# Performance work log

Measured on AMD Instinct MI355X. Metric: run time of the kernel, lower is better.

Reference implementation:

```python
import jax, jax.numpy as jnp
import numpy as np

EMBED_DIM = 512
KERNEL = 17


def setup_inputs() -> dict:
    key = jax.random.key(0)
    ks = jax.random.split(key, 5)
    B, L, C = 2, 8192, EMBED_DIM
    s = C ** -0.5
    x = jax.random.normal(ks[0], (B, L, C), dtype=jnp.float32)
    # weights stored as (in, out); equivalent to torch Linear weight.T
    w_qkv = jax.random.normal(ks[1], (C, 3 * C), dtype=jnp.float32) * s
    w_width = jax.random.normal(ks[2], (C, 1), dtype=jnp.float32) * s
    b_width = jax.random.normal(ks[3], (1,), dtype=jnp.float32) * 0.01
    w_out = jax.random.normal(ks[4], (C, C), dtype=jnp.float32) * s
    return {"x": x, "w_qkv": w_qkv, "w_width": w_width, "b_width": b_width, "w_out": w_out}


def reference(x, w_qkv, w_width, b_width, w_out):
    B, L, C = x.shape
    K = KERNEL
    half_k = K // 2
    scale = C ** -0.5

    qkv = x @ w_qkv                      # [B,L,3C]
    q, k, v = jnp.split(qkv, 3, axis=-1)

    # learned soft window width in [1, K]
    width = jax.nn.sigmoid(x @ w_width + b_width) * (K - 1) + 1.0   # [B,L,1]

    # sliding windows of k/v: pad along L then gather K-sized windows
    k_pad = jnp.pad(k, ((0, 0), (half_k, half_k), (0, 0)))
    v_pad = jnp.pad(v, ((0, 0), (half_k, half_k), (0, 0)))
    idx = jnp.arange(L)[:, None] + jnp.arange(K)[None, :]           # [L,K]
    k_win = k_pad[:, idx]                # [B,L,K,C]
    v_win = v_pad[:, idx]                # [B,L,K,C]

    scores = jnp.einsum('blc,blkc->blk', q, k_win) * scale          # [B,L,K]

    rel_pos = jnp.abs(jnp.arange(K, dtype=jnp.float32) - half_k)    # [K]
    soft_mask = jax.nn.sigmoid((width - rel_pos) * 5.0)             # [B,L,K]
    scores = scores - (1.0 - soft_mask) * 10000.0

    attn = jax.nn.softmax(scores, axis=-1)
    out = jnp.einsum('blk,blkc->blc', attn, v_win)                  # [B,L,C]
    return (out + v) @ w_out
```

## Files before the change

kernel.cpp:

```cpp
#include <hip/hip_runtime.h>

typedef unsigned short u16;
typedef unsigned int   u32;
typedef __attribute__((ext_vector_type(8))) short          shortx8;
typedef __attribute__((ext_vector_type(8))) unsigned short ushortx8;
typedef __attribute__((ext_vector_type(4))) float          floatx4;

#define AS1 __attribute__((address_space(1)))
#define AS3 __attribute__((address_space(3)))

#define SEG 8208
#define LV  16416

__device__ __forceinline__ float b2f(u16 v) {
  return __uint_as_float(((u32)v) << 16);
}
__device__ __forceinline__ u16 f2b(float f) {
  u32 u = __float_as_uint(f);
  u += 0x7FFF + ((u >> 16) & 1);
  return (u16)(u >> 16);
}
__device__ __forceinline__ void cp16(const void* g, void* l) {
  __builtin_amdgcn_global_load_lds((AS1 u32*)g, (AS3 u32*)l, 16, 0, 0);
}

__global__ void transpose_cast(const float* __restrict__ in, u16* __restrict__ out,
                               int R, int C) {
  __shared__ u16 tile[32][33];
  const int tx = threadIdx.x & 31;
  const int ty = threadIdx.x >> 5;
  const int cb = blockIdx.x * 32;
  const int rb = blockIdx.y * 32;
#pragma unroll
  for (int i = 0; i < 32; i += 8)
    tile[ty + i][tx] = f2b(in[(size_t)(rb + ty + i) * C + cb + tx]);
  __syncthreads();
#pragma unroll
  for (int i = 0; i < 32; i += 8)
    out[(size_t)(cb + ty + i) * R + rb + tx] = tile[tx][ty + i];
}

__global__ __launch_bounds__(256)
void cast_width(const float* __restrict__ x, const float* __restrict__ w_width,
                const float* __restrict__ b_width, u16* __restrict__ xb,
                float* __restrict__ width) {
  const int lane = threadIdx.x & 63;
  const int row  = blockIdx.x * 4 + (threadIdx.x >> 6);
  const float* xp = x + (size_t)row * 512 + lane * 8;
  floatx4 v0 = *(const floatx4*)xp;
  floatx4 v1 = *(const floatx4*)(xp + 4);
  floatx4 w0 = *(const floatx4*)(w_width + lane * 8);
  floatx4 w1 = *(const floatx4*)(w_width + lane * 8 + 4);
  float s = 0.f;
  ushortx8 o;
#pragma unroll
  for (int j = 0; j < 4; ++j) {
    s += v0[j] * w0[j] + v1[j] * w1[j];
    o[j] = f2b(v0[j]); o[4 + j] = f2b(v1[j]);
  }
  *(ushortx8*)(xb + (size_t)row * 512 + lane * 8) = o;
#pragma unroll
  for (int m = 32; m >= 1; m >>= 1) s += __shfl_xor(s, m, 64);
  if (lane == 0)
    width[row] = 16.f / (1.f + __expf(-(s + b_width[0]))) + 1.f;
}

__global__ void vt_zero_pad(u16* __restrict__ Vt) {
  const int idx = blockIdx.x * 256 + threadIdx.x;
  const int ch = idx >> 5;
  const int k  = idx & 31;
  const int seg = k >> 4;
  const int j   = k & 15;
  const int col = seg * SEG + (j < 8 ? j : 8192 + j);
  Vt[(size_t)ch * LV + col] = 0;
}

template <int MODE>
__global__ __launch_bounds__(256, 2)
void gemm_bt(const u16* __restrict__ A, const u16* __restrict__ Bt,
             void* __restrict__ C0, u16* __restrict__ Kb, u16* __restrict__ Vt) {
  const int K = 512;
  __shared__ alignas(16) u16 lds[17408];
  u16* As = lds;
  u16* Bs = lds + 8192;
  const int tid  = threadIdx.x;
  const int lane = tid & 63;
  const int wave = tid >> 6;
  const int quad = lane >> 4;
  const int lr   = lane & 15;
  const int row0 = blockIdx.x * 128;
  const int col0 = blockIdx.y * 128;
  const int wr   = (wave >> 1) * 64;
  const int wc   = (wave & 1) * 64;

  floatx4 acc[4][4];
#pragma unroll
  for (int i = 0; i < 4; ++i)
#pragma unroll
    for (int j = 0; j < 4; ++j) acc[i][j] = (floatx4)0.0f;

  int srow[4], scol[4];
#pragma unroll
  for (int p = 0; p < 4; ++p) {
    int c = p * 256 + tid;
    srow[p] = c >> 3;
    scol[p] = ((c & 7) ^ (srow[p] & 7)) * 8;
  }
  const int swz = lr & 7;

  for (int k0 = 0; k0 < K; k0 += 64) {
#pragma unroll
    for (int p = 0; p < 4; ++p)
      cp16(A + (size_t)(row0 + srow[p]) * K + k0 + scol[p], &As[(p * 256 + tid) * 8]);
#pragma unroll
    for (int p = 0; p < 4; ++p)
      cp16(Bt + (size_t)(col0 + srow[p]) * K + k0 + scol[p], &Bs[(p * 256 + tid) * 8]);
    __syncthreads();

#pragma unroll
    for (int ks = 0; ks < 2; ++ks) {
      shortx8 af[4], bf[4];
#pragma unroll
      for (int mi = 0; mi < 4; ++mi)
        af[mi] = *(const shortx8*)
            &As[((wr + mi * 16 + lr) * 8 + ((ks * 4 + quad) ^ swz)) * 8];
#pragma unroll
      for (int ni = 0; ni < 4; ++ni)
        bf[ni] = *(const shortx8*)
            &Bs[((wc + ni * 16 + lr) * 8 + ((ks * 4 + quad) ^ swz)) * 8];
#pragma unroll
      for (int mi = 0; mi < 4; ++mi)
#pragma unroll
        for (int ni = 0; ni < 4; ++ni)
          acc[mi][ni] = __builtin_amdgcn_mfma_f32_16x16x32_bf16(
              af[mi], bf[ni], acc[mi][ni], 0, 0, 0);
    }
    __syncthreads();
  }

  if constexpr (MODE == 1) {
    if (col0 < 1024) {
      u16* dst = (col0 < 512) ? (u16*)C0 : Kb;
      const int cb = col0 & 511;
#pragma unroll
      for (int mi = 0; mi < 4; ++mi)
#pragma unroll
        for (int ni = 0; ni < 4; ++ni)
#pragma unroll
          for (int r = 0; r < 4; ++r)
            lds[(wr + mi * 16 + quad * 4 + r) * 136 + wc + ni * 16 + lr] =
                f2b(acc[mi][ni][r]);
      __syncthreads();
      const int rr = tid >> 4, cc = (tid & 15) * 8;
#pragma unroll
      for (int it = 0; it < 8; ++it) {
        int row = it * 16 + rr;
        *(ushortx8*)(dst + (size_t)(row0 + row) * 512 + cb + cc) =
            *(const ushortx8*)&lds[row * 136 + cc];
      }
    } else {
      const int cb = col0 - 1024;
      const int bb = row0 >> 13, pib0 = row0 & 8191;
#pragma unroll
      for (int mi = 0; mi < 4; ++mi)
#pragma unroll
        for (int ni = 0; ni < 4; ++ni)
#pragma unroll
          for (int r = 0; r < 4; ++r)
            lds[(wc + ni * 16 + lr) * 136 + wr + mi * 16 + quad * 4 + r] =
                f2b(acc[mi][ni][r]);
      __syncthreads();
      const int rr = tid >> 4, cc = (tid & 15) * 8;
#pragma unroll
      for (int it = 0; it < 8; ++it) {
        int chl = it * 16 + rr;
        ushortx8 v = *(const ushortx8*)&lds[chl * 136 + cc];
        *(ushortx8*)(Vt + (size_t)(cb + chl) * LV + (size_t)bb * SEG + 8 + pib0 + cc) = v;
      }
    }
  } else {
    float* Cf = (float*)C0;
#pragma unroll
    for (int mi = 0; mi < 4; ++mi)
#pragma unroll
      for (int ni = 0; ni < 4; ++ni)
#pragma unroll
        for (int r = 0; r < 4; ++r) {
          int row = row0 + wr + mi * 16 + quad * 4 + r;
          int col = col0 + wc + ni * 16 + lr;
          Cf[(size_t)row * 512 + col] = acc[mi][ni][r];
        }
  }
}

__global__ __launch_bounds__(256)
void attn_mfma(const u16* __restrict__ Q, const u16* __restrict__ Kb,
               const u16* __restrict__ Vt, const float* __restrict__ width,
               u16* __restrict__ Out) {
  __shared__ float Sp[8][16][16];
  __shared__ u16   P[16][32];
  __shared__ u16   O[4][16][128];
  const int tid  = threadIdx.x;
  const int lane = tid & 63;
  const int wave = tid >> 6;
  const int quad = lane >> 4;
  const int lr   = lane & 15;
  const int p0   = blockIdx.x * 16;
  const int pib0 = p0 & 8191;
  const int bb   = p0 >> 13;

  floatx4 s0 = (floatx4)0.0f, s1 = (floatx4)0.0f;
#pragma unroll
  for (int s = 0; s < 4; ++s) {
    const int k0 = wave * 128 + s * 32 + quad * 8;
    shortx8 af = *(const shortx8*)(Q  + (size_t)(p0 + lr) * 512 + k0);
    shortx8 f0 = *(const shortx8*)(Kb + (ptrdiff_t)(p0 - 8 + lr) * 512 + k0);
    shortx8 f1 = *(const shortx8*)(Kb + (ptrdiff_t)(p0 + 8 + lr) * 512 + k0);
    s0 = __builtin_amdgcn_mfma_f32_16x16x32_bf16(af, f0, s0, 0, 0, 0);
    s1 = __builtin_amdgcn_mfma_f32_16x16x32_bf16(af, f1, s1, 0, 0, 0);
  }
#pragma unroll
  for (int r = 0; r < 4; ++r) {
    Sp[wave * 2 + 0][quad * 4 + r][lr] = s0[r];
    Sp[wave * 2 + 1][quad * 4 + r][lr] = s1[r];
  }
  __syncthreads();

  {
    const int row = tid >> 4, cg = tid & 15;
    const float scale = 0.044194173824159216f;
    const float wrow  = width[p0 + row];
    float sv[2]; float mx = -1e30f;
#pragma unroll
    for (int t = 0; t < 2; ++t) {
      const int col = t * 16 + cg;
      float s = Sp[t][row][cg] + Sp[2 + t][row][cg] +
                Sp[4 + t][row][cg] + Sp[6 + t][row][cg];
      const int d  = col - row;
      const int jb = pib0 + col - 8;
      const bool inband  = (d >= 0) && (d <= 16);
      const bool inbatch = ((unsigned)jb < 8192u);
      float rel  = fabsf((float)(d - 8));
      float mask = 1.f / (1.f + __expf(-5.f * (wrow - rel)));
      float pen  = (1.f - mask) * 10000.f;
      float val  = inband ? ((inbatch ? s * scale : 0.f) - pen) : -1e30f;
      sv[t] = val;
      mx = fmaxf(mx, val);
    }
#pragma unroll
    for (int m = 8; m >= 1; m >>= 1) mx = fmaxf(mx, __shfl_xor(mx, m, 64));
    float e0 = __expf(sv[0] - mx), e1 = __expf(sv[1] - mx);
    float sum = e0 + e1;
#pragma unroll
    for (int m = 8; m >= 1; m >>= 1) sum += __shfl_xor(sum, m, 64);
    const float inv = 1.f / sum;
    P[row][cg]      = f2b(e0 * inv + ((cg - row) == 8 ? 1.f : 0.f));
    P[row][cg + 16] = f2b(e1 * inv + ((cg + 16 - row) == 8 ? 1.f : 0.f));
  }
  __syncthreads();

  shortx8 pf = *(const shortx8*)&P[lr][quad * 8];
  const size_t cb0 = (size_t)bb * SEG + pib0;
#pragma unroll
  for (int ct = 0; ct < 8; ++ct) {
    const int ch = wave * 128 + ct * 16 + lr;
    shortx8 vf = *(const shortx8*)(Vt + (size_t)ch * LV + cb0 + quad * 8);
    floatx4 o = __builtin_amdgcn_mfma_f32_16x16x32_bf16(pf, vf, (floatx4)0.0f,
                                                        0, 0, 0);
#pragma unroll
    for (int r = 0; r < 4; ++r)
      O[wave][quad * 4 + r][ct * 16 + lr] = f2b(o[r]);
  }
  __syncthreads();
  {
    const int orow = lane >> 2;
#pragma unroll
    for (int i = 0; i < 4; ++i) {
      const int c = i * 32 + (lane & 3) * 8;
      ushortx8 v = *(const ushortx8*)&O[wave][orow][c];
      *(ushortx8*)(Out + (size_t)(p0 + orow) * 512 + wave * 128 + c) = v;
    }
  }
}

extern "C" void kernel_launch(void* const* d_in, const int* in_sizes, int n_in,
                              void* d_out, int out_size, void* d_ws, size_t ws_size,
                              hipStream_t stream) {
  const float* x       = (const float*)d_in[0];
  const float* w_qkv   = (const float*)d_in[1];
  const float* w_width = (const float*)d_in[2];
  const float* b_width = (const float*)d_in[3];
  const float* w_out   = (const float*)d_in[4];
  float* out = (float*)d_out;

  const int M = 16384, C = 512, N3 = 1536;
  char* ws = (char*)d_ws;
  u16*   xb    = (u16*)(ws);
  u16*   Qb    = (u16*)(ws + 16777216);
  u16*   Kb    = (u16*)(ws + 33554432 + 8192);
  u16*   Vt    = (u16*)(ws + 50348032);
  u16*   wqkvT = (u16*)(ws + 67158016);
  u16*   woutT = (u16*)(ws + 68730880);
  float* width = (float*)(ws + 69255168);

  dim3 blk(256);
  vt_zero_pad<<<dim3(64), blk, 0, stream>>>(Vt);
  cast_width<<<dim3(M / 4), blk, 0, stream>>>(x, w_width, b_width, xb, width);
  transpose_cast<<<dim3(N3 / 32, C / 32), blk, 0, stream>>>(w_qkv, wqkvT, C, N3);
  transpose_cast<<<dim3(C / 32, C / 32), blk, 0, stream>>>(w_out, woutT, C, C);
  gemm_bt<1><<<dim3(M / 128, N3 / 128), blk, 0, stream>>>(xb, wqkvT, Qb, Kb, Vt);
  attn_mfma<<<dim3(M / 16), blk, 0, stream>>>(Qb, Kb, Vt, width, Qb);
  gemm_bt<2><<<dim3(M / 128, C / 128), blk, 0, stream>>>(Qb, woutT, out, nullptr, nullptr);
}
```

Measured before the change: 160.5 us.

## Fuse prep kernels, raise GEMM occupancy, compute attention scores per-wave redundantly

Merges the zero-pad, cast/width, and two weight transpose kernels into one launch to cut launch overhead. Raises the GEMM launch bound to 4 blocks per CU, which may force register spills. In attention, each wave now computes the full 512-channel QK scores itself and does the softmax in registers with shuffles. This removes the cross-wave LDS reduction and one barrier, but quadruples the QK loads and MFMAs, and it pads the LDS arrays to avoid bank conflicts.

After: 165.4 us. 3.0% more time.

```diff
diff --git a/kernel.cpp b/kernel.cpp
--- a/kernel.cpp
+++ b/kernel.cpp
@@ -24,59 +24,63 @@
   __builtin_amdgcn_global_load_lds((AS1 u32*)g, (AS3 u32*)l, 16, 0, 0);
 }
 
-__global__ void transpose_cast(const float* __restrict__ in, u16* __restrict__ out,
-                               int R, int C) {
+__global__ __launch_bounds__(256)
+void prep(const float* __restrict__ x, const float* __restrict__ w_width,
+          const float* __restrict__ b_width, const float* __restrict__ w_qkv,
+          const float* __restrict__ w_out, u16* __restrict__ xb,
+          float* __restrict__ width, u16* __restrict__ wqkvT,
+          u16* __restrict__ woutT, u16* __restrict__ Vt) {
   __shared__ u16 tile[32][33];
-  const int tx = threadIdx.x & 31;
-  const int ty = threadIdx.x >> 5;
-  const int cb = blockIdx.x * 32;
-  const int rb = blockIdx.y * 32;
-#pragma unroll
-  for (int i = 0; i < 32; i += 8)
-    tile[ty + i][tx] = f2b(in[(size_t)(rb + ty + i) * C + cb + tx]);
-  __syncthreads();
-#pragma unroll
-  for (int i = 0; i < 32; i += 8)
-    out[(size_t)(cb + ty + i) * R + rb + tx] = tile[tx][ty + i];
-}
-
-__global__ __launch_bounds__(256)
-void cast_width(const float* __restrict__ x, const float* __restrict__ w_width,
-                const float* __restrict__ b_width, u16* __restrict__ xb,
-                float* __restrict__ width) {
-  const int lane = threadIdx.x & 63;
-  const int row  = blockIdx.x * 4 + (threadIdx.x >> 6);
-  const float* xp = x + (size_t)row * 512 + lane * 8;
-  floatx4 v0 = *(const floatx4*)xp;
-  floatx4 v1 = *(const floatx4*)(xp + 4);
-  floatx4 w0 = *(const floatx4*)(w_width + lane * 8);
-  floatx4 w1 = *(const floatx4*)(w_width + lane * 8 + 4);
-  float s = 0.f;
-  ushortx8 o;
-#pragma unroll
-  for (int j = 0; j < 4; ++j) {
-    s += v0[j] * w0[j] + v1[j] * w1[j];
-    o[j] = f2b(v0[j]); o[4 + j] = f2b(v1[j]);
-  }
-  *(ushortx8*)(xb + (size_t)row * 512 + lane * 8) = o;
-#pragma unroll
-  for (int m = 32; m >= 1; m >>= 1) s += __shfl_xor(s, m, 64);
-  if (lane == 0)
-    width[row] = 16.f / (1.f + __expf(-(s + b_width[0]))) + 1.f;
-}
-
-__global__ void vt_zero_pad(u16* __restrict__ Vt) {
-  const int idx = blockIdx.x * 256 + threadIdx.x;
-  const int ch = idx >> 5;
-  const int k  = idx & 31;
-  const int seg = k >> 4;
-  const int j   = k & 15;
-  const int col = seg * SEG + (j < 8 ? j : 8192 + j);
-  Vt[(size_t)ch * LV + col] = 0;
+  const int b = blockIdx.x;
+  if (b < 4096) {
+    const int lane = threadIdx.x & 63;
+    const int row  = b * 4 + (threadIdx.x >> 6);
+    const float* xp = x + (size_t)row * 512 + lane * 8;
+    floatx4 v0 = *(const floatx4*)xp;
+    floatx4 v1 = *(const floatx4*)(xp + 4);
+    floatx4 w0 = *(const floatx4*)(w_width + lane * 8);
+    floatx4 w1 = *(const floatx4*)(w_width + lane * 8 + 4);
+    float s = 0.f;
+    ushortx8 o;
+#pragma unroll
+    for (int j = 0; j < 4; ++j) {
+      s += v0[j] * w0[j] + v1[j] * w1[j];
+      o[j] = f2b(v0[j]); o[4 + j] = f2b(v1[j]);
+    }
+    *(ushortx8*)(xb + (size_t)row * 512 + lane * 8) = o;
+#pragma unroll
+    for (int m = 32; m >= 1; m >>= 1) s += __shfl_xor(s, m, 64);
+    if (lane == 0)
+      width[row] = 16.f / (1.f + __expf(-(s + b_width[0]))) + 1.f;
+  } else if (b < 5120) {
+    const float* in; u16* out; int R, C, t;
+    if (b < 4864) { in = w_qkv; out = wqkvT; R = 512; C = 1536; t = b - 4096; }
+    else          { in = w_out; out = woutT; R = 512; C = 512;  t = b - 4864; }
+    const int nbx = C / 32;
+    const int cb = (t % nbx) * 32;
+    const int rb = (t / nbx) * 32;
+    const int tx = threadIdx.x & 31;
+    const int ty = threadIdx.x >> 5;
+#pragma unroll
+    for (int i = 0; i < 32; i += 8)
+      tile[ty + i][tx] = f2b(in[(size_t)(rb + ty + i) * C + cb + tx]);
+    __syncthreads();
+#pragma unroll
+    for (int i = 0; i < 32; i += 8)
+      out[(size_t)(cb + ty + i) * R + rb + tx] = tile[tx][ty + i];
+  } else {
+    const int idx = (b - 5120) * 256 + threadIdx.x;
+    const int ch = idx >> 5;
+    const int k  = idx & 31;
+    const int seg = k >> 4;
+    const int j   = k & 15;
+    const int col = seg * SEG + (j < 8 ? j : 8192 + j);
+    Vt[(size_t)ch * LV + col] = 0;
+  }
 }
 
 template <int MODE>
-__global__ __launch_bounds__(256, 2)
+__global__ __launch_bounds__(256, 4)
 void gemm_bt(const u16* __restrict__ A, const u16* __restrict__ Bt,
              void* __restrict__ C0, u16* __restrict__ Kb, u16* __restrict__ Vt) {
   const int K = 512;
@@ -197,9 +201,8 @@
 void attn_mfma(const u16* __restrict__ Q, const u16* __restrict__ Kb,
                const u16* __restrict__ Vt, const float* __restrict__ width,
                u16* __restrict__ Out) {
-  __shared__ float Sp[8][16][16];
-  __shared__ u16   P[16][32];
-  __shared__ u16   O[4][16][128];
+  __shared__ u16 P[4][16][40];
+  __shared__ u16 O[4][16][136];
   const int tid  = threadIdx.x;
   const int lane = tid & 63;
   const int wave = tid >> 6;
@@ -211,55 +214,68 @@
 
   floatx4 s0 = (floatx4)0.0f, s1 = (floatx4)0.0f;
 #pragma unroll
-  for (int s = 0; s < 4; ++s) {
-    const int k0 = wave * 128 + s * 32 + quad * 8;
+  for (int s = 0; s < 16; ++s) {
+    const int k0 = s * 32 + quad * 8;
     shortx8 af = *(const shortx8*)(Q  + (size_t)(p0 + lr) * 512 + k0);
     shortx8 f0 = *(const shortx8*)(Kb + (ptrdiff_t)(p0 - 8 + lr) * 512 + k0);
     shortx8 f1 = *(const shortx8*)(Kb + (ptrdiff_t)(p0 + 8 + lr) * 512 + k0);
     s0 = __builtin_amdgcn_mfma_f32_16x16x32_bf16(af, f0, s0, 0, 0, 0);
     s1 = __builtin_amdgcn_mfma_f32_16x16x32_bf16(af, f1, s1, 0, 0, 0);
   }
+
+  const float scale = 0.044194173824159216f;
+  float v0[4], v1[4], mx[4];
 #pragma unroll
   for (int r = 0; r < 4; ++r) {
-    Sp[wave * 2 + 0][quad * 4 + r][lr] = s0[r];
-    Sp[wave * 2 + 1][quad * 4 + r][lr] = s1[r];
-  }
-  __syncthreads();
-
-  {
-    const int row = tid >> 4, cg = tid & 15;
-    const float scale = 0.044194173824159216f;
-    const float wrow  = width[p0 + row];
-    float sv[2]; float mx = -1e30f;
-#pragma unroll
-    for (int t = 0; t < 2; ++t) {
-      const int col = t * 16 + cg;
-      float s = Sp[t][row][cg] + Sp[2 + t][row][cg] +
-                Sp[4 + t][row][cg] + Sp[6 + t][row][cg];
-      const int d  = col - row;
-      const int jb = pib0 + col - 8;
-      const bool inband  = (d >= 0) && (d <= 16);
+    const int row = quad * 4 + r;
+    const float wrow = width[p0 + row];
+    {
+      const int d  = lr - row;
+      const int jb = pib0 + lr - 8;
+      const bool inband  = (d >= 0);
       const bool inbatch = ((unsigned)jb < 8192u);
       float rel  = fabsf((float)(d - 8));
       float mask = 1.f / (1.f + __expf(-5.f * (wrow - rel)));
       float pen  = (1.f - mask) * 10000.f;
-      float val  = inband ? ((inbatch ? s * scale : 0.f) - pen) : -1e30f;
-      sv[t] = val;
-      mx = fmaxf(mx, val);
-    }
-#pragma unroll
-    for (int m = 8; m >= 1; m >>= 1) mx = fmaxf(mx, __shfl_xor(mx, m, 64));
-    float e0 = __expf(sv[0] - mx), e1 = __expf(sv[1] - mx);
-    float sum = e0 + e1;
-#pragma unroll
-    for (int m = 8; m >= 1; m >>= 1) sum += __shfl_xor(sum, m, 64);
-    const float inv = 1.f / sum;
-    P[row][cg]      = f2b(e0 * inv + ((cg - row) == 8 ? 1.f : 0.f));
-    P[row][cg + 16] = f2b(e1 * inv + ((cg + 16 - row) == 8 ? 1.f : 0.f));
+      v0[r] = inband ? ((inbatch ? s0[r] * scale : 0.f) - pen) : -1e30f;
+    }
+    {
+      const int d  = lr + 16 - row;
+      const int jb = pib0 + lr + 8;
+      const bool inband  = (d <= 16);
+      const bool inbatch = ((unsigned)jb < 8192u);
+      float rel  = fabsf((float)(d - 8));
+      float mask = 1.f / (1.f + __expf(-5.f * (wrow - rel)));
+      float pen  = (1.f - mask) * 10000.f;
+      v1[r] = inband ? ((inbatch ? s1[r] * scale : 0.f) - pen) : -1e30f;
+    }
+    mx[r] = fmaxf(v0[r], v1[r]);
+  }
+#pragma unroll
+  for (int m = 8; m >= 1; m >>= 1)
+#pragma unroll
+    for (int r = 0; r < 4; ++r) mx[r] = fmaxf(mx[r], __shfl_xor(mx[r], m, 64));
+  float e0[4], e1[4], sum[4];
+#pragma unroll
+  for (int r = 0; r < 4; ++r) {
+    e0[r] = __expf(v0[r] - mx[r]);
+    e1[r] = __expf(v1[r] - mx[r]);
+    sum[r] = e0[r] + e1[r];
+  }
+#pragma unroll
+  for (int m = 8; m >= 1; m >>= 1)
+#pragma unroll
+    for (int r = 0; r < 4; ++r) sum[r] += __shfl_xor(sum[r], m, 64);
+#pragma unroll
+  for (int r = 0; r < 4; ++r) {
+    const int row = quad * 4 + r;
+    const float inv = 1.f / sum[r];
+    P[wave][row][lr]      = f2b(e0[r] * inv + ((lr - row) == 8 ? 1.f : 0.f));
+    P[wave][row][lr + 16] = f2b(e1[r] * inv + ((lr + 16 - row) == 8 ? 1.f : 0.f));
   }
   __syncthreads();
 
-  shortx8 pf = *(const shortx8*)&P[lr][quad * 8];
+  shortx8 pf = *(const shortx8*)&P[wave][lr][quad * 8];
   const size_t cb0 = (size_t)bb * SEG + pib0;
 #pragma unroll
   for (int ct = 0; ct < 8; ++ct) {
@@ -304,10 +320,8 @@
   float* width = (float*)(ws + 69255168);
 
   dim3 blk(256);
-  vt_zero_pad<<<dim3(64), blk, 0, stream>>>(Vt);
-  cast_width<<<dim3(M / 4), blk, 0, stream>>>(x, w_width, b_width, xb, width);
-  transpose_cast<<<dim3(N3 / 32, C / 32), blk, 0, stream>>>(w_qkv, wqkvT, C, N3);
-  transpose_cast<<<dim3(C / 32, C / 32), blk, 0, stream>>>(w_out, woutT, C, C);
+  prep<<<dim3(5184), blk, 0, stream>>>(x, w_width, b_width, w_qkv, w_out,
+                                       xb, width, wqkvT, woutT, Vt);
   gemm_bt<1><<<dim3(M / 128, N3 / 128), blk, 0, stream>>>(xb, wqkvT, Qb, Kb, Vt);
   attn_mfma<<<dim3(M / 16), blk, 0, stream>>>(Qb, Kb, Vt, width, Qb);
   gemm_bt<2><<<dim3(M / 128, C / 128), blk, 0, stream>>>(Qb, woutT, out, nullptr, nullptr);
```

## Fuse prep kernels into one launch, raise GEMM occupancy, pad attention LDS

Applied to the files above, without the earlier changes.

Merges the four preprocessing kernels (Vt zero-padding, x cast plus width, and both weight transpose-casts) into one launch that picks its branch by block index. This removes three kernel launches and the gaps between them. The GEMM launch bound minimum-blocks hint rises from 2 to 3 to push occupancy, which may constrain register allocation. The attention output LDS buffer row is padded from 128 to 136 elements to reduce bank conflicts.

New measurement: 152.4 us, median of 2. -5.1%, faster.

```diff
diff --git a/kernel.cpp b/kernel.cpp
--- a/kernel.cpp
+++ b/kernel.cpp
@@ -24,59 +24,63 @@
   __builtin_amdgcn_global_load_lds((AS1 u32*)g, (AS3 u32*)l, 16, 0, 0);
 }
 
-__global__ void transpose_cast(const float* __restrict__ in, u16* __restrict__ out,
-                               int R, int C) {
+__global__ __launch_bounds__(256)
+void prep(const float* __restrict__ x, const float* __restrict__ w_width,
+          const float* __restrict__ b_width, const float* __restrict__ w_qkv,
+          const float* __restrict__ w_out, u16* __restrict__ xb,
+          float* __restrict__ width, u16* __restrict__ wqkvT,
+          u16* __restrict__ woutT, u16* __restrict__ Vt) {
   __shared__ u16 tile[32][33];
-  const int tx = threadIdx.x & 31;
-  const int ty = threadIdx.x >> 5;
-  const int cb = blockIdx.x * 32;
-  const int rb = blockIdx.y * 32;
-#pragma unroll
-  for (int i = 0; i < 32; i += 8)
-    tile[ty + i][tx] = f2b(in[(size_t)(rb + ty + i) * C + cb + tx]);
-  __syncthreads();
-#pragma unroll
-  for (int i = 0; i < 32; i += 8)
-    out[(size_t)(cb + ty + i) * R + rb + tx] = tile[tx][ty + i];
-}
-
-__global__ __launch_bounds__(256)
-void cast_width(const float* __restrict__ x, const float* __restrict__ w_width,
-                const float* __restrict__ b_width, u16* __restrict__ xb,
-                float* __restrict__ width) {
-  const int lane = threadIdx.x & 63;
-  const int row  = blockIdx.x * 4 + (threadIdx.x >> 6);
-  const float* xp = x + (size_t)row * 512 + lane * 8;
-  floatx4 v0 = *(const floatx4*)xp;
-  floatx4 v1 = *(const floatx4*)(xp + 4);
-  floatx4 w0 = *(const floatx4*)(w_width + lane * 8);
-  floatx4 w1 = *(const floatx4*)(w_width + lane * 8 + 4);
-  float s = 0.f;
-  ushortx8 o;
-#pragma unroll
-  for (int j = 0; j < 4; ++j) {
-    s += v0[j] * w0[j] + v1[j] * w1[j];
-    o[j] = f2b(v0[j]); o[4 + j] = f2b(v1[j]);
-  }
-  *(ushortx8*)(xb + (size_t)row * 512 + lane * 8) = o;
-#pragma unroll
-  for (int m = 32; m >= 1; m >>= 1) s += __shfl_xor(s, m, 64);
-  if (lane == 0)
-    width[row] = 16.f / (1.f + __expf(-(s + b_width[0]))) + 1.f;
-}
-
-__global__ void vt_zero_pad(u16* __restrict__ Vt) {
-  const int idx = blockIdx.x * 256 + threadIdx.x;
-  const int ch = idx >> 5;
-  const int k  = idx & 31;
-  const int seg = k >> 4;
-  const int j   = k & 15;
-  const int col = seg * SEG + (j < 8 ? j : 8192 + j);
-  Vt[(size_t)ch * LV + col] = 0;
+  const int b = blockIdx.x;
+  if (b < 4096) {
+    const int lane = threadIdx.x & 63;
+    const int row  = b * 4 + (threadIdx.x >> 6);
+    const float* xp = x + (size_t)row * 512 + lane * 8;
+    floatx4 v0 = *(const floatx4*)xp;
+    floatx4 v1 = *(const floatx4*)(xp + 4);
+    floatx4 w0 = *(const floatx4*)(w_width + lane * 8);
+    floatx4 w1 = *(const floatx4*)(w_width + lane * 8 + 4);
+    float s = 0.f;
+    ushortx8 o;
+#pragma unroll
+    for (int j = 0; j < 4; ++j) {
+      s += v0[j] * w0[j] + v1[j] * w1[j];
+      o[j] = f2b(v0[j]); o[4 + j] = f2b(v1[j]);
+    }
+    *(ushortx8*)(xb + (size_t)row * 512 + lane * 8) = o;
+#pragma unroll
+    for (int m = 32; m >= 1; m >>= 1) s += __shfl_xor(s, m, 64);
+    if (lane == 0)
+      width[row] = 16.f / (1.f + __expf(-(s + b_width[0]))) + 1.f;
+  } else if (b < 5120) {
+    const float* in; u16* out; int R, C, t;
+    if (b < 4864) { in = w_qkv; out = wqkvT; R = 512; C = 1536; t = b - 4096; }
+    else          { in = w_out; out = woutT; R = 512; C = 512;  t = b - 4864; }
+    const int nbx = C / 32;
+    const int cb = (t % nbx) * 32;
+    const int rb = (t / nbx) * 32;
+    const int tx = threadIdx.x & 31;
+    const int ty = threadIdx.x >> 5;
+#pragma unroll
+    for (int i = 0; i < 32; i += 8)
+      tile[ty + i][tx] = f2b(in[(size_t)(rb + ty + i) * C + cb + tx]);
+    __syncthreads();
+#pragma unroll
+    for (int i = 0; i < 32; i += 8)
+      out[(size_t)(cb + ty + i) * R + rb + tx] = tile[tx][ty + i];
+  } else {
+    const int idx = (b - 5120) * 256 + threadIdx.x;
+    const int ch = idx >> 5;
+    const int k  = idx & 31;
+    const int seg = k >> 4;
+    const int j   = k & 15;
+    const int col = seg * SEG + (j < 8 ? j : 8192 + j);
+    Vt[(size_t)ch * LV + col] = 0;
+  }
 }
 
 template <int MODE>
-__global__ __launch_bounds__(256, 2)
+__global__ __launch_bounds__(256, 3)
 void gemm_bt(const u16* __restrict__ A, const u16* __restrict__ Bt,
              void* __restrict__ C0, u16* __restrict__ Kb, u16* __restrict__ Vt) {
   const int K = 512;
@@ -199,7 +203,7 @@
                u16* __restrict__ Out) {
   __shared__ float Sp[8][16][16];
   __shared__ u16   P[16][32];
-  __shared__ u16   O[4][16][128];
+  __shared__ u16   O[4][16][136];
   const int tid  = threadIdx.x;
   const int lane = tid & 63;
   const int wave = tid >> 6;
@@ -304,10 +308,8 @@
   float* width = (float*)(ws + 69255168);
 
   dim3 blk(256);
-  vt_zero_pad<<<dim3(64), blk, 0, stream>>>(Vt);
-  cast_width<<<dim3(M / 4), blk, 0, stream>>>(x, w_width, b_width, xb, width);
-  transpose_cast<<<dim3(N3 / 32, C / 32), blk, 0, stream>>>(w_qkv, wqkvT, C, N3);
-  transpose_cast<<<dim3(C / 32, C / 32), blk, 0, stream>>>(w_out, woutT, C, C);
+  prep<<<dim3(5184), blk, 0, stream>>>(x, w_width, b_width, w_qkv, w_out,
+                                       xb, width, wqkvT, woutT, Vt);
   gemm_bt<1><<<dim3(M / 128, N3 / 128), blk, 0, stream>>>(xb, wqkvT, Qb, Kb, Vt);
   attn_mfma<<<dim3(M / 16), blk, 0, stream>>>(Qb, Kb, Vt, width, Qb);
   gemm_bt<2><<<dim3(M / 128, C / 128), blk, 0, stream>>>(Qb, woutT, out, nullptr, nullptr);
```
